# Performance work log

Hardware: AMD Instinct MI355X
Metric: run time of the kernel (lower is better)

The kernel has to match this reference:

```python
import jax, jax.numpy as jnp
import numpy as np

EMBED_DIM = 64
HEAD_NUM = 16
BS, QL, KL = 4, 2048, 2048


def setup_inputs() -> dict:
    key = jax.random.key(0)
    k1, k2, k3, k4, k5, k6, k7, k8 = jax.random.split(key, 8)
    d, H = EMBED_DIM, HEAD_NUM
    q_origin = jax.random.normal(k1, (BS, QL, d), dtype=jnp.float32)
    k_origin = jax.random.normal(k2, (BS, KL, d), dtype=jnp.float32)
    mask = jax.random.randint(k3, (BS, QL, KL), 0, 2).astype(bool)
    scale = 1.0 / np.sqrt(d)
    Wq = jax.random.normal(k4, (d, d * H), dtype=jnp.float32) * scale
    Wk = jax.random.normal(k5, (d, d * H), dtype=jnp.float32) * scale
    Wv = jax.random.normal(k6, (d, d * H), dtype=jnp.float32) * scale
    Wfc = jax.random.normal(k7, (d, d), dtype=jnp.float32) * scale
    bfc = jax.random.normal(k8, (d,), dtype=jnp.float32) * 0.01
    return {"q_origin": q_origin, "k_origin": k_origin, "mask": mask,
            "Wq": Wq, "Wk": Wk, "Wv": Wv, "Wfc": Wfc, "bfc": bfc}


def reference(q_origin, k_origin, mask, Wq, Wk, Wv, Wfc, bfc):
    bs, ql, d = q_origin.shape
    _, kl, _ = k_origin.shape
    H = Wq.shape[1] // d
    # projections, split into H heads of width d
    q = (q_origin @ Wq).reshape(bs, ql, H, d)   # bqhd
    k = (k_origin @ Wk).reshape(bs, kl, H, d)   # bkhd
    v = (k_origin @ Wv).reshape(bs, kl, H, d)   # bkhd
    scores = jnp.einsum('bqhd,bkhd->bhqk', q, k)
    scores = jnp.where(mask[:, None, :, :], -jnp.inf, scores)
    attn = jax.nn.softmax(scores / jnp.sqrt(jnp.asarray(d, scores.dtype)), axis=-1)
    attn = jnp.nan_to_num(attn)
    out = jnp.einsum('bhqk,bkhd->bqhd', attn, v)
    # torch code concatenates heads along the sequence axis: (bs, ql*H, d)
    out = out.reshape(bs, ql * H, d)
    return jnp.tanh(out @ Wfc + bfc)
```

## Files before the change

kernel.cpp:

```cpp
#include <hip/hip_runtime.h>
#include <hip/hip_bf16.h>

#define BSZ 4
#define SEQ 2048
#define NH  16
#define DH  64
#define TOK (BSZ*SEQ)
#define PROJC (NH*DH)

typedef __bf16 bf16x8 __attribute__((ext_vector_type(8)));
typedef float  f32x4  __attribute__((ext_vector_type(4)));
typedef float  f32x16 __attribute__((ext_vector_type(16)));
typedef unsigned int uint4v __attribute__((ext_vector_type(4)));
typedef unsigned int uint2v __attribute__((ext_vector_type(2)));

__device__ inline unsigned short f2bf(float f) {
    __bf16 h = (__bf16)f;
    return __builtin_bit_cast(unsigned short, h);
}

__device__ inline bf16x8 ld8(const unsigned short* p) {
    return __builtin_bit_cast(bf16x8, *reinterpret_cast<const uint4v*>(p));
}

__device__ inline float fexp2(float x) {
    float r;
    asm("v_exp_f32 %0, %1" : "=v"(r) : "v"(x));
    return r;
}

__device__ inline void gload16(const unsigned short* g, unsigned short* l) {
    __builtin_amdgcn_global_load_lds(
        (__attribute__((address_space(1))) void*)g,
        (__attribute__((address_space(3))) void*)l, 16, 0, 0);
}

__global__ __launch_bounds__(256) void prep_kernel(const float* __restrict__ q,
                                                   const float* __restrict__ k,
                                                   const float* __restrict__ Wq,
                                                   const float* __restrict__ Wk,
                                                   const float* __restrict__ Wv,
                                                   const float* __restrict__ Wfc,
                                                   unsigned short* __restrict__ qbf,
                                                   unsigned short* __restrict__ kbf,
                                                   unsigned short* __restrict__ WqT,
                                                   unsigned short* __restrict__ WkT,
                                                   unsigned short* __restrict__ WvT,
                                                   unsigned short* __restrict__ WfcT) {
    int bx = blockIdx.x;
    if (bx < 4096) {
        int idx = (bx & 2047) * 256 + threadIdx.x;
        if (bx < 2048) qbf[idx] = f2bf(q[idx]);
        else           kbf[idx] = f2bf(k[idx]);
        return;
    }
    bx -= 4096;
    const float* W; unsigned short* WT; int cols; int base;
    if      (bx < 256) { W = Wq;  WT = WqT;  cols = PROJC; base = bx; }
    else if (bx < 512) { W = Wk;  WT = WkT;  cols = PROJC; base = bx - 256; }
    else if (bx < 768) { W = Wv;  WT = WvT;  cols = PROJC; base = bx - 512; }
    else               { W = Wfc; WT = WfcT; cols = 64;    base = bx - 768; }
    int idx = base * 256 + threadIdx.x;
    int c = idx % cols, kk = idx / cols;
    WT[c * 64 + kk] = f2bf(W[kk * cols + c]);
}

__global__ __launch_bounds__(256) void maskpack_kernel(const int* __restrict__ mask,
                                                       unsigned long long* __restrict__ mbits) {
    size_t gid = (size_t)blockIdx.x * 256 + threadIdx.x;
    int lane = threadIdx.x & 63;
    unsigned long long bal = __ballot(mask[gid] != 0);
    if (lane == 0) mbits[gid >> 6] = bal;
}

__global__ __launch_bounds__(256) void proj_kernel(const unsigned short* __restrict__ qbf,
                                                   const unsigned short* __restrict__ kbf,
                                                   const unsigned short* __restrict__ WqT,
                                                   const unsigned short* __restrict__ WkT,
                                                   const unsigned short* __restrict__ WvT,
                                                   unsigned short* __restrict__ Qo,
                                                   unsigned short* __restrict__ Ko,
                                                   unsigned short* __restrict__ Vto) {
    int z = blockIdx.z;
    const unsigned short* A  = (z == 0) ? qbf : kbf;
    const unsigned short* WT = (z == 0) ? WqT : (z == 1) ? WkT : WvT;
    int tid = threadIdx.x, w = tid >> 6, lane = tid & 63;
    int l15 = lane & 15, l4 = lane >> 4;
    int r0 = blockIdx.x * 64 + w * 16;
    int c0 = blockIdx.y * 64;
    int h = blockIdx.y;
    int b = r0 >> 11;
    size_t bh = (size_t)(b * NH + h);

    const unsigned short* ap = A + (r0 + l15) * 64 + l4 * 8;
    bf16x8 a0 = ld8(ap), a1 = ld8(ap + 32);

    for (int ct = 0; ct < 4; ++ct) {
        const unsigned short* wp = WT + (c0 + ct * 16 + l15) * 64 + l4 * 8;
        bf16x8 b0 = ld8(wp), b1 = ld8(wp + 32);
        f32x4 acc = {0.f, 0.f, 0.f, 0.f};
        if (z == 2) {
            acc = __builtin_amdgcn_mfma_f32_16x16x32_bf16(a0, b0, acc, 0, 0, 0);
            acc = __builtin_amdgcn_mfma_f32_16x16x32_bf16(a1, b1, acc, 0, 0, 0);
        } else {
            acc = __builtin_amdgcn_mfma_f32_16x16x32_bf16(b0, a0, acc, 0, 0, 0);
            acc = __builtin_amdgcn_mfma_f32_16x16x32_bf16(b1, a1, acc, 0, 0, 0);
        }
        uint2v pk;
        pk.x = (unsigned)f2bf(acc[0]) | ((unsigned)f2bf(acc[1]) << 16);
        pk.y = (unsigned)f2bf(acc[2]) | ((unsigned)f2bf(acc[3]) << 16);
        if (z == 2) {
            int dd = ct * 16 + l15;
            int q0 = (r0 + l4 * 4) & 2047;
            *reinterpret_cast<uint2v*>(Vto + (bh * 64 + dd) * SEQ + q0) = pk;
        } else {
            int qq = (r0 + l15) & 2047;
            unsigned short* dst = (z == 0) ? Qo : Ko;
            *reinterpret_cast<uint2v*>(dst + (bh * SEQ + qq) * 64 + ct * 16 + l4 * 4) = pk;
        }
    }
}

__global__ __launch_bounds__(256, 4) void attn_kernel(const unsigned short* __restrict__ Q,
                                                      const unsigned short* __restrict__ K,
                                                      const unsigned short* __restrict__ Vt,
                                                      const unsigned long long* __restrict__ mbits,
                                                      unsigned short* __restrict__ O) {
    __shared__ __align__(16) unsigned short Ks[2][64 * 64];
    __shared__ __align__(16) unsigned short Vs[2][64 * 64];
    int tid = threadIdx.x, w = tid >> 6, lane = tid & 63;
    int l31 = lane & 31, hi = lane >> 5;
    int hi4 = hi * 4;

    int bid = blockIdx.x;
    int swz = (bid & 7) * 128 + (bid >> 3);
    int bh = swz >> 4;
    int qt = swz & 15;
    int b = bh >> 4;
    int qbase = qt * 128 + w * 32;

    const unsigned short* Qh = Q  + (size_t)bh * SEQ * 64;
    const unsigned short* Kh = K  + (size_t)bh * SEQ * 64;
    const unsigned short* Vh = Vt + (size_t)bh * 64 * SEQ;
    const unsigned long long* mrow =
        mbits + ((size_t)b * SEQ + qbase + l31) * (SEQ / 64);

    int row1 = (w << 3) + (lane >> 3);
    int row2 = row1 + 32;
    int sc1 = (lane & 7) ^ (row1 & 7);
    unsigned short* Kd0 = &Ks[0][0] + w * 512;
    unsigned short* Vd0 = &Vs[0][0] + w * 512;
    unsigned short* Kd1 = &Ks[1][0] + w * 512;
    unsigned short* Vd1 = &Vs[1][0] + w * 512;

    bf16x8 qf[4];
    #pragma unroll
    for (int s = 0; s < 4; ++s)
        qf[s] = ld8(Qh + (size_t)(qbase + l31) * 64 + s * 16 + hi * 8);

    bf16x8 ones;
    #pragma unroll
    for (int i = 0; i < 8; ++i) ones[i] = (__bf16)1.0f;

    f32x16 o0 = {0.f,0.f,0.f,0.f,0.f,0.f,0.f,0.f,0.f,0.f,0.f,0.f,0.f,0.f,0.f,0.f};
    f32x16 o1 = o0;
    f32x16 ellD = o0;
    const float C = 0.125f * 1.44269504088896f;

    gload16(Kh + (size_t)row1 * 64 + sc1 * 8, Kd0);
    gload16(Kh + (size_t)row2 * 64 + sc1 * 8, Kd0 + 2048);
    gload16(Vh + (size_t)row1 * SEQ + sc1 * 8, Vd0);
    gload16(Vh + (size_t)row2 * SEQ + sc1 * 8, Vd0 + 2048);
    __syncthreads();

    int cur = 0;
    for (int kb = 0; kb < SEQ; kb += 64) {
        if (kb + 64 < SEQ) {
            int nkb = kb + 64;
            unsigned short* Kd = cur ? Kd0 : Kd1;
            unsigned short* Vd = cur ? Vd0 : Vd1;
            gload16(Kh + (size_t)(nkb + row1) * 64 + sc1 * 8, Kd);
            gload16(Kh + (size_t)(nkb + row2) * 64 + sc1 * 8, Kd + 2048);
            gload16(Vh + (size_t)row1 * SEQ + nkb + sc1 * 8, Vd);
            gload16(Vh + (size_t)row2 * SEQ + nkb + sc1 * 8, Vd + 2048);
        }
        unsigned long long wb = mrow[kb >> 6];
        const unsigned short* Kc = &Ks[cur][0];
        const unsigned short* Vc = &Vs[cur][0];

        #pragma unroll
        for (int kt = 0; kt < 2; ++kt) {
            f32x16 z = {0.f,0.f,0.f,0.f,0.f,0.f,0.f,0.f,0.f,0.f,0.f,0.f,0.f,0.f,0.f,0.f};
            int krow = kt * 32 + l31;
            #pragma unroll
            for (int s = 0; s < 4; ++s) {
                const unsigned short* kp =
                    Kc + krow * 64 + ((((s << 1) + hi) ^ (krow & 7)) << 3);
                z = __builtin_amdgcn_mfma_f32_32x32x16_bf16(ld8(kp), qf[s], z, 0, 0, 0);
            }
            unsigned wsh = (unsigned)(wb >> (kt * 32)) >> hi4;
            unsigned wpk[8];
            #pragma unroll
            for (int rq = 0; rq < 4; ++rq) {
                #pragma unroll
                for (int rr = 0; rr < 2; ++rr) {
                    float e[2];
                    #pragma unroll
                    for (int j = 0; j < 2; ++j) {
                        int pos = rq * 8 + 2 * rr + j;
                        int sx = (int)(wsh << (31 - pos)) >> 31;
                        float bias = __builtin_bit_cast(float, (unsigned)sx & 0xFF800000u);
                        e[j] = fexp2(__builtin_fmaf(z[rq * 4 + 2 * rr + j], C, bias));
                    }
                    wpk[rq * 2 + rr] = (unsigned)f2bf(e[0]) | ((unsigned)f2bf(e[1]) << 16);
                }
            }
            __builtin_amdgcn_s_setprio(1);
            #pragma unroll
            for (int sl = 0; sl < 2; ++sl) {
                uint4v aw = {wpk[sl * 4 + 0], wpk[sl * 4 + 1],
                             wpk[sl * 4 + 2], wpk[sl * 4 + 3]};
                bf16x8 af = __builtin_bit_cast(bf16x8, aw);
                ellD = __builtin_amdgcn_mfma_f32_32x32x16_bf16(af, ones, ellD, 0, 0, 0);
                int n = kt * 2 + sl;
                {
                    int vrow = l31;
                    int c0i = ((2 * n) ^ (vrow & 7)) << 3;
                    int c1i = ((2 * n + 1) ^ (vrow & 7)) << 3;
                    uint2v lo = *reinterpret_cast<const uint2v*>(Vc + vrow * 64 + c0i + hi4);
                    uint2v hh = *reinterpret_cast<const uint2v*>(Vc + vrow * 64 + c1i + hi4);
                    uint4v vw = {lo.x, lo.y, hh.x, hh.y};
                    o0 = __builtin_amdgcn_mfma_f32_32x32x16_bf16(
                        af, __builtin_bit_cast(bf16x8, vw), o0, 0, 0, 0);
                }
                {
                    int vrow = 32 + l31;
                    int c0i = ((2 * n) ^ (vrow & 7)) << 3;
                    int c1i = ((2 * n + 1) ^ (vrow & 7)) << 3;
                    uint2v lo = *reinterpret_cast<const uint2v*>(Vc + vrow * 64 + c0i + hi4);
                    uint2v hh = *reinterpret_cast<const uint2v*>(Vc + vrow * 64 + c1i + hi4);
                    uint4v vw = {lo.x, lo.y, hh.x, hh.y};
                    o1 = __builtin_amdgcn_mfma_f32_32x32x16_bf16(
                        af, __builtin_bit_cast(bf16x8, vw), o1, 0, 0, 0);
                }
            }
            __builtin_amdgcn_s_setprio(0);
        }
        __syncthreads();
        cur ^= 1;
    }
    #pragma unroll
    for (int reg = 0; reg < 16; ++reg) {
        float l = ellD[reg];
        float rcp = (l == 0.f) ? 0.f : __builtin_amdgcn_rcpf(l);
        int ql = (reg & 3) + 8 * (reg >> 2) + hi4;
        size_t base = ((size_t)bh * SEQ + qbase + ql) * 64 + l31;
        O[base]      = f2bf(o0[reg] * rcp);
        O[base + 32] = f2bf(o1[reg] * rcp);
    }
}

__global__ __launch_bounds__(256) void fc_kernel(const unsigned short* __restrict__ O,
                                                 const unsigned short* __restrict__ WfcT,
                                                 const float* __restrict__ bfc,
                                                 float* __restrict__ out) {
    int tid = threadIdx.x, w = tid >> 6, lane = tid & 63;
    int l15 = lane & 15, l4 = lane >> 4;
    int r0 = blockIdx.x * 64 + w * 16;

    int row = r0 + l15;
    int h = row & 15, t_ = row >> 4;
    int q = t_ & 2047, b = t_ >> 11;
    const unsigned short* op = O + (((size_t)(b * NH + h)) * SEQ + q) * 64 + l4 * 8;
    bf16x8 a0 = ld8(op), a1 = ld8(op + 32);

    for (int ct = 0; ct < 4; ++ct) {
        const unsigned short* wp = WfcT + (ct * 16 + l15) * 64 + l4 * 8;
        bf16x8 b0 = ld8(wp), b1 = ld8(wp + 32);
        f32x4 acc = {0.f, 0.f, 0.f, 0.f};
        acc = __builtin_amdgcn_mfma_f32_16x16x32_bf16(b0, a0, acc, 0, 0, 0);
        acc = __builtin_amdgcn_mfma_f32_16x16x32_bf16(b1, a1, acc, 0, 0, 0);
        f32x4 bv = *reinterpret_cast<const f32x4*>(bfc + ct * 16 + l4 * 4);
        f32x4 st;
        #pragma unroll
        for (int r = 0; r < 4; ++r) {
            float x = acc[r] + bv[r];
            x = fminf(fmaxf(x, -9.f), 9.f);
            float t = fexp2(x * 2.88539008177793f);
            st[r] = (t - 1.f) * __builtin_amdgcn_rcpf(t + 1.f);
        }
        *reinterpret_cast<f32x4*>(out + (size_t)row * 64 + ct * 16 + l4 * 4) = st;
    }
}

extern "C" void kernel_launch(void* const* d_in, const int* in_sizes, int n_in,
                              void* d_out, int out_size, void* d_ws, size_t ws_size,
                              hipStream_t stream) {
    const float* q_origin = (const float*)d_in[0];
    const float* k_origin = (const float*)d_in[1];
    const int*   mask     = (const int*)d_in[2];
    const float* Wq       = (const float*)d_in[3];
    const float* Wk       = (const float*)d_in[4];
    const float* Wv       = (const float*)d_in[5];
    const float* Wfc      = (const float*)d_in[6];
    const float* bfc      = (const float*)d_in[7];
    float* out = (float*)d_out;

    unsigned short* ws = (unsigned short*)d_ws;
    unsigned short* qbf  = ws;
    unsigned short* kbf  = qbf  + TOK * DH;
    unsigned short* WqT  = kbf  + TOK * DH;
    unsigned short* WkT  = WqT  + 64 * PROJC;
    unsigned short* WvT  = WkT  + 64 * PROJC;
    unsigned short* WfcT = WvT  + 64 * PROJC;
    unsigned short* Qb   = WfcT + 64 * 64;
    unsigned short* Kb   = Qb   + (size_t)BSZ * NH * SEQ * DH;
    unsigned short* Vtb  = Kb   + (size_t)BSZ * NH * SEQ * DH;
    unsigned short* Ob   = Vtb  + (size_t)BSZ * NH * SEQ * DH;
    unsigned long long* mbits = (unsigned long long*)d_ws;

    prep_kernel<<<4880, 256, 0, stream>>>(q_origin, k_origin, Wq, Wk, Wv, Wfc,
                                          qbf, kbf, WqT, WkT, WvT, WfcT);
    proj_kernel<<<dim3(TOK / 64, PROJC / 64, 3), 256, 0, stream>>>(
        qbf, kbf, WqT, WkT, WvT, Qb, Kb, Vtb);
    maskpack_kernel<<<(size_t)BSZ * SEQ * SEQ / 256, 256, 0, stream>>>(mask, mbits);
    attn_kernel<<<1024, 256, 0, stream>>>(Qb, Kb, Vtb, mbits, Ob);
    fc_kernel<<<(size_t)BSZ * SEQ * NH / 64, 256, 0, stream>>>(Ob, WfcT, bfc, out);
}
```

Baseline: 187.6 us.

## Stage projection outputs through LDS for coalesced stores; unroll attention double-buffer loop

The projection kernel now writes its MFMA results into a padded shared-memory tile and then emits 16-byte coalesced stores for Q, K and the transposed V, replacing the scattered 8-byte stores. The attention kernel's ping-pong loop is unrolled by two, so buffer selection is static and the per-iteration cur toggle and branch go away. This costs an extra LDS round trip and barrier in the projection kernel and some code growth in attention.

```diff
diff --git a/kernel.cpp b/kernel.cpp
--- a/kernel.cpp
+++ b/kernel.cpp
@@ -81,6 +81,7 @@
                                                    unsigned short* __restrict__ Qo,
                                                    unsigned short* __restrict__ Ko,
                                                    unsigned short* __restrict__ Vto) {
+    __shared__ __align__(16) unsigned short T[64][72];
     int z = blockIdx.z;
     const unsigned short* A  = (z == 0) ? qbf : kbf;
     const unsigned short* WT = (z == 0) ? WqT : (z == 1) ? WkT : WvT;
@@ -88,13 +89,13 @@
     int l15 = lane & 15, l4 = lane >> 4;
     int r0 = blockIdx.x * 64 + w * 16;
     int c0 = blockIdx.y * 64;
-    int h = blockIdx.y;
-    int b = r0 >> 11;
-    size_t bh = (size_t)(b * NH + h);
+    int b = blockIdx.x >> 5;
+    size_t bh = (size_t)(b * NH + blockIdx.y);
 
     const unsigned short* ap = A + (r0 + l15) * 64 + l4 * 8;
     bf16x8 a0 = ld8(ap), a1 = ld8(ap + 32);
 
+    #pragma unroll
     for (int ct = 0; ct < 4; ++ct) {
         const unsigned short* wp = WT + (c0 + ct * 16 + l15) * 64 + l4 * 8;
         bf16x8 b0 = ld8(wp), b1 = ld8(wp + 32);
@@ -110,13 +111,29 @@
         pk.x = (unsigned)f2bf(acc[0]) | ((unsigned)f2bf(acc[1]) << 16);
         pk.y = (unsigned)f2bf(acc[2]) | ((unsigned)f2bf(acc[3]) << 16);
         if (z == 2) {
-            int dd = ct * 16 + l15;
-            int q0 = (r0 + l4 * 4) & 2047;
-            *reinterpret_cast<uint2v*>(Vto + (bh * 64 + dd) * SEQ + q0) = pk;
+            *reinterpret_cast<uint2v*>(&T[ct * 16 + l15][w * 16 + l4 * 4]) = pk;
         } else {
-            int qq = (r0 + l15) & 2047;
-            unsigned short* dst = (z == 0) ? Qo : Ko;
-            *reinterpret_cast<uint2v*>(dst + (bh * SEQ + qq) * 64 + ct * 16 + l4 * 4) = pk;
+            *reinterpret_cast<uint2v*>(&T[w * 16 + l15][ct * 16 + l4 * 4]) = pk;
+        }
+    }
+    __syncthreads();
+
+    int rl8 = tid >> 3, chunk = tid & 7;
+    int q0 = (blockIdx.x & 31) * 64;
+    if (z == 2) {
+        #pragma unroll
+        for (int p = 0; p < 2; ++p) {
+            int dd = p * 32 + rl8;
+            uint4v v = *reinterpret_cast<const uint4v*>(&T[dd][chunk * 8]);
+            *reinterpret_cast<uint4v*>(Vto + (bh * 64 + dd) * SEQ + q0 + chunk * 8) = v;
+        }
+    } else {
+        unsigned short* dst = (z == 0) ? Qo : Ko;
+        #pragma unroll
+        for (int p = 0; p < 2; ++p) {
+            int rl = p * 32 + rl8;
+            uint4v v = *reinterpret_cast<const uint4v*>(&T[rl][chunk * 8]);
+            *reinterpret_cast<uint4v*>(dst + (bh * SEQ + q0 + rl) * 64 + chunk * 8) = v;
         }
     }
 }
@@ -167,27 +184,15 @@
     f32x16 ellD = o0;
     const float C = 0.125f * 1.44269504088896f;
 
-    gload16(Kh + (size_t)row1 * 64 + sc1 * 8, Kd0);
-    gload16(Kh + (size_t)row2 * 64 + sc1 * 8, Kd0 + 2048);
-    gload16(Vh + (size_t)row1 * SEQ + sc1 * 8, Vd0);
-    gload16(Vh + (size_t)row2 * SEQ + sc1 * 8, Vd0 + 2048);
-    __syncthreads();
-
-    int cur = 0;
-    for (int kb = 0; kb < SEQ; kb += 64) {
-        if (kb + 64 < SEQ) {
-            int nkb = kb + 64;
-            unsigned short* Kd = cur ? Kd0 : Kd1;
-            unsigned short* Vd = cur ? Vd0 : Vd1;
-            gload16(Kh + (size_t)(nkb + row1) * 64 + sc1 * 8, Kd);
-            gload16(Kh + (size_t)(nkb + row2) * 64 + sc1 * 8, Kd + 2048);
-            gload16(Vh + (size_t)row1 * SEQ + nkb + sc1 * 8, Vd);
-            gload16(Vh + (size_t)row2 * SEQ + nkb + sc1 * 8, Vd + 2048);
-        }
+    auto stage_tile = [&](unsigned short* Kd, unsigned short* Vd, int nkb) {
+        gload16(Kh + (size_t)(nkb + row1) * 64 + sc1 * 8, Kd);
+        gload16(Kh + (size_t)(nkb + row2) * 64 + sc1 * 8, Kd + 2048);
+        gload16(Vh + (size_t)row1 * SEQ + nkb + sc1 * 8, Vd);
+        gload16(Vh + (size_t)row2 * SEQ + nkb + sc1 * 8, Vd + 2048);
+    };
+
+    auto compute_tile = [&](const unsigned short* Kc, const unsigned short* Vc, int kb) {
         unsigned long long wb = mrow[kb >> 6];
-        const unsigned short* Kc = &Ks[cur][0];
-        const unsigned short* Vc = &Vs[cur][0];
-
         #pragma unroll
         for (int kt = 0; kt < 2; ++kt) {
             f32x16 z = {0.f,0.f,0.f,0.f,0.f,0.f,0.f,0.f,0.f,0.f,0.f,0.f,0.f,0.f,0.f,0.f};
@@ -246,8 +251,18 @@
             }
             __builtin_amdgcn_s_setprio(0);
         }
+    };
+
+    stage_tile(Kd0, Vd0, 0);
+    __syncthreads();
+
+    for (int kb = 0; kb < SEQ; kb += 128) {
+        stage_tile(Kd1, Vd1, kb + 64);
+        compute_tile(&Ks[0][0], &Vs[0][0], kb);
         __syncthreads();
-        cur ^= 1;
+        if (kb + 128 < SEQ) stage_tile(Kd0, Vd0, kb + 128);
+        compute_tile(&Ks[1][0], &Vs[1][0], kb + 64);
+        __syncthreads();
     }
     #pragma unroll
     for (int reg = 0; reg < 16; ++reg) {
```

Measured after the change: 183.2 us. 2.4% less time.
